# Performance work log

Hardware: AMD Instinct MI355X
Metric: run time of the kernel (lower is better)

Reference implementation:

```python
import jax, jax.numpy as jnp
import numpy as np

B, S, H = 2, 2048, 2048
NH, NKV, HD = 32, 8, 64
GROUPS = NH // NKV
SCALE = HD ** -0.5


def _rope_tables(key):
    # Real RoPE cos/sin tables (HF Llama style), shape [B, S, HD]
    inv_freq = 1.0 / (10000.0 ** (jnp.arange(0, HD, 2, dtype=jnp.float32) / HD))  # [HD/2]
    t = jnp.arange(S, dtype=jnp.float32)
    freqs = jnp.outer(t, inv_freq)                      # [S, HD/2]
    emb = jnp.concatenate([freqs, freqs], axis=-1)      # [S, HD]
    cos = jnp.broadcast_to(jnp.cos(emb)[None], (B, S, HD))
    sin = jnp.broadcast_to(jnp.sin(emb)[None], (B, S, HD))
    return cos, sin


def setup_inputs() -> dict:
    key = jax.random.key(0)
    ks = jax.random.split(key, 9)
    w = 0.02
    cos, sin = _rope_tables(key)
    return {
        "hidden_states": jax.random.normal(ks[0], (B, S, H), jnp.float32),
        "bounding_box_embeddings": jax.random.normal(ks[1], (B, S, H), jnp.float32),
        "cos": cos,
        "sin": sin,
        "Wq": jax.random.normal(ks[2], (H, NH * HD), jnp.float32) * w,
        "Wk": jax.random.normal(ks[3], (H, NKV * HD), jnp.float32) * w,
        "Wv": jax.random.normal(ks[4], (H, NKV * HD), jnp.float32) * w,
        "Wo": jax.random.normal(ks[5], (NH * HD, H), jnp.float32) * w,
        "Wsq": jax.random.normal(ks[6], (H, NH * HD), jnp.float32) * w,
        "Wsk": jax.random.normal(ks[7], (H, NKV * HD), jnp.float32) * w,
    }


def _rotate_half(x):
    x1, x2 = x[..., : HD // 2], x[..., HD // 2 :]
    return jnp.concatenate([-x2, x1], axis=-1)


def _apply_rope(q, k, cos, sin):
    # q: [B,NH,S,HD], k: [B,NKV,S,HD]; cos/sin [B,S,HD] -> broadcast over heads
    c = cos[:, None, :, :]
    s = sin[:, None, :, :]
    return q * c + _rotate_half(q) * s, k * c + _rotate_half(k) * s


def _proj_heads(x, W, n_heads):
    b, s, _ = x.shape
    return (x @ W).reshape(b, s, n_heads, HD).transpose(0, 2, 1, 3)  # [B,nh,S,HD]


def reference(hidden_states, bounding_box_embeddings, cos, sin, Wq, Wk, Wv, Wo, Wsq, Wsk):
    # Text Q/K/V with RoPE
    q = _proj_heads(hidden_states, Wq, NH)
    k = _proj_heads(hidden_states, Wk, NKV)
    v = _proj_heads(hidden_states, Wv, NKV)
    q, k = _apply_rope(q, k, cos, sin)
    # Spatial Q/K (no V) with RoPE
    sq = _proj_heads(bounding_box_embeddings, Wsq, NH)
    sk = _proj_heads(bounding_box_embeddings, Wsk, NKV)
    sq, sk = _apply_rope(sq, sk, cos, sin)
    # Fused text+spatial states, then GQA repeat_kv
    q = q + sq                                   # [B,NH,S,HD]
    k = jnp.repeat(k + sk, GROUPS, axis=1)       # [B,NH,S,HD]
    v = jnp.repeat(v, GROUPS, axis=1)            # [B,NH,S,HD]
    # Eager attention with causal mask
    scores = jnp.einsum("bhqd,bhkd->bhqk", q, k) * SCALE
    causal = jnp.tril(jnp.ones((S, S), dtype=bool))
    scores = jnp.where(causal[None, None], scores, jnp.finfo(jnp.float32).min)
    probs = jax.nn.softmax(scores.astype(jnp.float32), axis=-1).astype(q.dtype)
    attn = jnp.einsum("bhqk,bhkd->bhqd", probs, v)           # [B,NH,S,HD]
    attn = attn.transpose(0, 2, 1, 3).reshape(B, S, NH * HD)  # [B,S,NH*HD]
    return attn @ Wo
```

## Files before the change

### kernel.cpp

```cpp
#include <hip/hip_runtime.h>

#define B_ 2
#define S_ 2048
#define H_ 2048
#define NH_ 32
#define NKV_ 8
#define HD_ 64

typedef short short8 __attribute__((ext_vector_type(8)));
typedef float f32x4 __attribute__((ext_vector_type(4)));
typedef float f32x16 __attribute__((ext_vector_type(16)));
typedef unsigned int uint4v __attribute__((ext_vector_type(4)));

__device__ __forceinline__ float bf2f(unsigned short u) {
  union { unsigned int i; float f; } v; v.i = ((unsigned int)u) << 16; return v.f;
}
__device__ __forceinline__ unsigned short f2bf(float f) {
  union { float f; unsigned int i; } v; v.f = f;
  unsigned int u = v.i;
  u += 0x7fffu + ((u >> 16) & 1u);
  return (unsigned short)(u >> 16);
}
__device__ __forceinline__ unsigned int cvtpk(float lo, float hi) {
  unsigned int r;
  asm("v_cvt_pk_bf16_f32 %0, %1, %2" : "=v"(r) : "v"(lo), "v"(hi));
  return r;
}
__device__ __forceinline__ void pl32swap(unsigned int& a, unsigned int& b) {
  asm("v_permlane32_swap_b32 %0, %1" : "+v"(a), "+v"(b));
}
__device__ __forceinline__ short8 mkfrag(unsigned a, unsigned b, unsigned c, unsigned d) {
  union { uint4v u; short8 s; } x;
  x.u = (uint4v){a, b, c, d};
  return x.s;
}
__device__ __forceinline__ void gload_lds16(const unsigned short* g, unsigned short* l) {
  __builtin_amdgcn_global_load_lds((const __attribute__((address_space(1))) void*)g,
                                   (__attribute__((address_space(3))) void*)l,
                                   16, 0, 0);
}
#define MFMA32(A, B, C) __builtin_amdgcn_mfma_f32_32x32x16_bf16(A, B, C, 0, 0, 0)
#define BARF() asm volatile("s_barrier" ::: "memory")

__global__ __launch_bounds__(256) void castA_frag(const float* __restrict__ in,
                                                  unsigned short* __restrict__ out) {
  int c = blockIdx.x * 4 + (threadIdx.x >> 6);
  int l = threadIdx.x & 63;
  int D = c & 31, KT = (c >> 5) & 31, bm = c >> 10;
  int row = bm * 256 + ((D >> 4) & 1) * 128 + ((D >> 3) & 1) * 64 + ((D >> 1) & 3) * 16 + (l & 15);
  int k = KT * 64 + (D & 1) * 32 + (l >> 4) * 8;
  const float* src = in + (size_t)row * 2048 + k;
  float4 v0 = *(const float4*)src;
  float4 v1 = *(const float4*)(src + 4);
  ushort4 o0, o1;
  o0.x = f2bf(v0.x); o0.y = f2bf(v0.y); o0.z = f2bf(v0.z); o0.w = f2bf(v0.w);
  o1.x = f2bf(v1.x); o1.y = f2bf(v1.y); o1.z = f2bf(v1.z); o1.w = f2bf(v1.w);
  unsigned short* dst = out + (size_t)c * 512 + l * 8;
  *(ushort4*)dst = o0;
  *(ushort4*)(dst + 4) = o1;
}

__global__ __launch_bounds__(256) void castW_frag(const float* __restrict__ W0,
                                                  const float* __restrict__ W1,
                                                  const float* __restrict__ W2,
                                                  unsigned short* __restrict__ out) {
  __shared__ float tile[64][33];
  int c = blockIdx.x;
  int ngroup = c & 7, KT = (c >> 3) & 31, bn = c >> 8;
  int n0 = bn * 256 + ngroup * 32;
  const float* W; int Nw, nb;
  if (n0 < 2048)      { W = W0; Nw = 2048; nb = n0; }
  else if (n0 < 2560) { W = W1; Nw = 512;  nb = n0 - 2048; }
  else                { W = W2; Nw = 512;  nb = n0 - 2560; }
  int t = threadIdx.x;
  int col = t & 31, r8 = t >> 5;
#pragma unroll
  for (int p = 0; p < 8; ++p) {
    int kk = p * 8 + r8;
    tile[kk][col] = W[(size_t)(KT * 64 + kk) * Nw + nb + col];
  }
  __syncthreads();
  int e = t >> 6, l = t & 63;
  int nf = e >> 1, ks = e & 1;
  ushort4 o0, o1;
  unsigned short* op = (unsigned short*)&o0;
#pragma unroll
  for (int j = 0; j < 8; ++j) {
    unsigned short v = f2bf(tile[ks * 32 + (l >> 4) * 8 + j][nf * 16 + (l & 15)]);
    if (j < 4) op[j] = v; else ((unsigned short*)&o1)[j - 4] = v;
  }
  unsigned short* dst = out + (((size_t)(c >> 3) * 32 + ngroup * 4 + e) << 9) + l * 8;
  *(ushort4*)dst = o0;
  *(ushort4*)(dst + 4) = o1;
}

__global__ __launch_bounds__(256) void vtrans_kernel(const unsigned short* __restrict__ P1,
                                                     unsigned short* __restrict__ Vt) {
  __shared__ unsigned short tile[32][33];
  int s0 = blockIdx.x * 32, d0 = blockIdx.y * 32, bk = blockIdx.z;
  int b = bk >> 3, kv = bk & 7;
  int tx = threadIdx.x & 31, ty = threadIdx.x >> 5;
#pragma unroll
  for (int i = 0; i < 32; i += 8)
    tile[ty + i][tx] = P1[(size_t)(b * S_ + s0 + ty + i) * 3072 + 2560 + kv * 64 + d0 + tx];
  __syncthreads();
#pragma unroll
  for (int i = 0; i < 32; i += 8)
    Vt[(size_t)(bk * 64 + d0 + ty + i) * S_ + s0 + tx] = tile[tx][ty + i];
}

__global__ __launch_bounds__(256) void combine_rope(const unsigned short* __restrict__ P1,
                                                    const unsigned short* __restrict__ P2,
                                                    const float* __restrict__ cosT,
                                                    const float* __restrict__ sinT,
                                                    unsigned short* __restrict__ Qb,
                                                    unsigned short* __restrict__ Kb) {
  int id = blockIdx.x * 256 + threadIdx.x;
  int row = id / 640;
  int grp = id - row * 640;
  int b = row >> 11;
  int s = row & 2047;
  bool isQ = grp < 512;
  int n = isQ ? grp * 4 : (grp - 512) * 4;
  int h = n >> 6;
  int d = n & 63;
  int base = isQ ? 0 : 2048;
  const int ld1 = 3072, ld2 = 2560;
  int pd = (d < 32) ? d + 32 : d - 32;
  float sign = (d < 32) ? -1.f : 1.f;
  int pcol = base + h * 64 + pd;

  ushort4 a1 = *(const ushort4*)&P1[(size_t)row * ld1 + base + n];
  ushort4 a2 = *(const ushort4*)&P2[(size_t)row * ld2 + base + n];
  ushort4 b1 = *(const ushort4*)&P1[(size_t)row * ld1 + pcol];
  ushort4 b2 = *(const ushort4*)&P2[(size_t)row * ld2 + pcol];
  float4 cv = *(const float4*)&cosT[(size_t)row * 64 + d];
  float4 sv = *(const float4*)&sinT[(size_t)row * 64 + d];
  float scale = isQ ? 0.125f : 1.0f;

  float xs[4] = { bf2f(a1.x) + bf2f(a2.x), bf2f(a1.y) + bf2f(a2.y),
                  bf2f(a1.z) + bf2f(a2.z), bf2f(a1.w) + bf2f(a2.w) };
  float xp[4] = { bf2f(b1.x) + bf2f(b2.x), bf2f(b1.y) + bf2f(b2.y),
                  bf2f(b1.z) + bf2f(b2.z), bf2f(b1.w) + bf2f(b2.w) };
  float cc[4] = { cv.x, cv.y, cv.z, cv.w };
  float ss[4] = { sv.x, sv.y, sv.z, sv.w };
  ushort4 o;
  unsigned short* op = (unsigned short*)&o;
#pragma unroll
  for (int i = 0; i < 4; ++i)
    op[i] = f2bf((xs[i] * cc[i] + sign * xp[i] * ss[i]) * scale);

  if (isQ)
    *(ushort4*)&Qb[((size_t)(b * NH_ + h) * S_ + s) * HD_ + d] = o;
  else
    *(ushort4*)&Kb[((size_t)(b * NKV_ + h) * S_ + s) * HD_ + d] = o;
}

#define RD_A(BC, MH) do { \
  _Pragma("unroll") for (int mf = 0; mf < 4; ++mf) { \
    _Pragma("unroll") for (int ks = 0; ks < 2; ++ks) \
      a[mf][ks] = *(const short8*)&lds[BC][((wm * 2 + (MH)) * 8 + mf * 2 + ks) * 512 + l * 8]; \
  } \
} while (0)

#define RD_B(BC, NH, DST) do { \
  _Pragma("unroll") for (int nf = 0; nf < 2; ++nf) { \
    _Pragma("unroll") for (int ks = 0; ks < 2; ++ks) \
      DST[nf][ks] = *(const short8*)&lds[BC][16384 + (((wn * 2 + (NH)) * 2 + nf) * 2 + ks) * 512 + l * 8]; \
  } \
} while (0)

#define MM(MH, NH, BB) do { \
  _Pragma("unroll") for (int mf = 0; mf < 4; ++mf) { \
    _Pragma("unroll") for (int nf = 0; nf < 2; ++nf) { \
      _Pragma("unroll") for (int ks = 0; ks < 2; ++ks) \
        acc[(MH) * 4 + mf][(NH) * 2 + nf] = __builtin_amdgcn_mfma_f32_16x16x32_bf16( \
            a[mf][ks], BB[nf][ks], acc[(MH) * 4 + mf][(NH) * 2 + nf], 0, 0, 0); \
    } \
  } \
} while (0)

#define STAGE_A(H, KT) do { \
  int bq_ = (KT) & 1; \
  int d1_ = (H) * 8 + w; \
  gload_lds16(aF + (((size_t)((KT) * 32 + d1_)) << 9), &lds[bq_][d1_ * 512]); \
  gload_lds16(aF + (((size_t)((KT) * 32 + 16 + d1_)) << 9), &lds[bq_][(16 + d1_) * 512]); \
} while (0)

#define STAGE_B(H, KT) do { \
  int bq_ = (KT) & 1; \
  int e1_ = (w >> 2) * 8 + (H) * 4 + (w & 3); \
  gload_lds16(bF + (((size_t)((KT) * 32 + e1_)) << 9), &lds[bq_][16384 + e1_ * 512]); \
  gload_lds16(bF + (((size_t)((KT) * 32 + 16 + e1_)) << 9), &lds[bq_][16384 + (16 + e1_) * 512]); \
} while (0)

#define GROUP_P(BC, G) do { \
  int kt1 = (G) + 1; if (kt1 > 31) kt1 = 31; \
  int kt2 = (G) + 2; if (kt2 > 31) kt2 = 31; \
  int BN_ = kt1 & 1; \
  BARF(); \
  __builtin_amdgcn_s_setprio(1); MM(0, 0, b0); __builtin_amdgcn_s_setprio(0); \
  RD_B(BC, 1, b1); \
  STAGE_A(1, kt1); \
  BARF(); \
  __builtin_amdgcn_s_setprio(1); MM(0, 1, b1); __builtin_amdgcn_s_setprio(0); \
  STAGE_A(0, kt2); \
  BARF(); \
  RD_A(BC, 1); \
  __builtin_amdgcn_s_setprio(1); MM(1, 0, b0); __builtin_amdgcn_s_setprio(0); \
  STAGE_B(0, kt2); \
  asm volatile("s_waitcnt vmcnt(8)" ::: "memory"); \
  BARF(); \
  __builtin_amdgcn_s_setprio(1); MM(1, 1, b1); __builtin_amdgcn_s_setprio(0); \
  RD_A(BN_, 0); \
  RD_B(BN_, 0, b0); \
  STAGE_B(1, kt2); \
  asm volatile("s_waitcnt vmcnt(6)" ::: "memory"); \
} while (0)

__global__ __launch_bounds__(512, 2) void gemm256(const unsigned short* __restrict__ Afr,
                                                  const unsigned short* __restrict__ Wfr,
                                                  void* __restrict__ Cv,
                                                  int N, int nbx) {
  __shared__ unsigned short lds[2][32768];
  int nwg = gridDim.x;
  int orig = blockIdx.x;
  int wgid = (orig & 7) * (nwg >> 3) + (orig >> 3);
  int bn = wgid % nbx, bm = wgid / nbx;
  int t = threadIdx.x, w = t >> 6, l = t & 63;
  int wm = w >> 2, wn = w & 3;

  const unsigned short* aF = Afr + ((size_t)bm << 19) + l * 8;
  const unsigned short* bF = Wfr + ((size_t)bn << 19) + l * 8;

  short8 a[4][2], b0[2][2], b1[2][2];
  f32x4 acc[8][4];
#pragma unroll
  for (int mi = 0; mi < 8; ++mi)
#pragma unroll
    for (int ni = 0; ni < 4; ++ni) acc[mi][ni] = 0.f;

  STAGE_A(0, 0); STAGE_A(1, 0); STAGE_B(0, 0); STAGE_B(1, 0);
  STAGE_A(0, 1); STAGE_B(0, 1); STAGE_B(1, 1);
  asm volatile("s_waitcnt vmcnt(6)" ::: "memory");
  BARF();
  RD_A(0, 0);
  RD_B(0, 0, b0);

  for (int tg = 0; tg < 32; tg += 2) {
    GROUP_P(0, tg);
    GROUP_P(1, tg + 1);
  }
  asm volatile("s_waitcnt vmcnt(0)" ::: "memory");

#pragma unroll
  for (int mi = 0; mi < 8; ++mi) {
    int row = bm * 256 + wm * 128 + (mi >> 2) * 64 + (mi & 3) * 16 + (l >> 4) * 4;
#pragma unroll
    for (int ni = 0; ni < 4; ++ni) {
      int col = bn * 256 + wn * 64 + (ni >> 1) * 32 + (ni & 1) * 16 + (l & 15);
#pragma unroll
      for (int r = 0; r < 4; ++r)
        ((unsigned short*)Cv)[(size_t)(row + r) * N + col] = f2bf(acc[mi][ni][r]);
    }
  }
}

#define RD_AO(BC) do { \
  _Pragma("unroll") for (int mf = 0; mf < 4; ++mf) { \
    _Pragma("unroll") for (int ks = 0; ks < 2; ++ks) \
      a[mf][ks] = *(const short8*)&lds3[BC][(wm * 8 + mf * 2 + ks) * 512 + l * 8]; \
  } \
} while (0)

#define RD_BO(BC, NH, DST) do { \
  _Pragma("unroll") for (int nf = 0; nf < 2; ++nf) { \
    _Pragma("unroll") for (int ks = 0; ks < 2; ++ks) \
      DST[nf][ks] = *(const short8*)&lds3[BC][8192 + (((wn * 2 + (NH)) * 2 + nf) * 2 + ks) * 512 + l * 8]; \
  } \
} while (0)

#define MM_O(NH, BB) do { \
  _Pragma("unroll") for (int mf = 0; mf < 4; ++mf) { \
    _Pragma("unroll") for (int nf = 0; nf < 2; ++nf) { \
      _Pragma("unroll") for (int ks = 0; ks < 2; ++ks) \
        acc[mf][(NH) * 2 + nf] = __builtin_amdgcn_mfma_f32_16x16x32_bf16( \
            a[mf][ks], BB[nf][ks], acc[mf][(NH) * 2 + nf], 0, 0, 0); \
    } \
  } \
} while (0)

#define STAGE_AO(KT) do { \
  int bq_ = (KT) & 1; \
  gload_lds16(aRM + (size_t)(KT) * 64, &lds3[bq_][w * 512]); \
  gload_lds16(aRM + (size_t)64 * 2048 + (size_t)(KT) * 64, &lds3[bq_][(8 + w) * 512]); \
} while (0)

#define STAGE_BO(H, KT) do { \
  int bq_ = (KT) & 1; \
  int e1_ = (w >> 2) * 8 + (H) * 4 + (w & 3); \
  gload_lds16(bF + (((size_t)((KT) * 32 + e1_)) << 9), &lds3[bq_][8192 + e1_ * 512]); \
  gload_lds16(bF + (((size_t)((KT) * 32 + 16 + e1_)) << 9), &lds3[bq_][8192 + (16 + e1_) * 512]); \
} while (0)

#define GROUPO(BC, G) do { \
  int kt1 = (G) + 1; if (kt1 > 31) kt1 = 31; \
  int kt2 = (G) + 2; if (kt2 > 31) kt2 = 31; \
  RD_AO(BC); RD_BO(BC, 0, b0); \
  STAGE_BO(1, kt1); \
  BARF(); \
  __builtin_amdgcn_s_setprio(1); MM_O(0, b0); __builtin_amdgcn_s_setprio(0); \
  BARF(); \
  RD_BO(BC, 1, b1); \
  STAGE_AO(kt2); STAGE_BO(0, kt2); \
  BARF(); \
  __builtin_amdgcn_s_setprio(1); MM_O(1, b1); __builtin_amdgcn_s_setprio(0); \
  asm volatile("s_waitcnt vmcnt(4)" ::: "memory"); \
  BARF(); \
} while (0)

__global__ __launch_bounds__(512, 2) void gemm_op(const unsigned short* __restrict__ Arm,
                                                  const unsigned short* __restrict__ Wfr,
                                                  float* __restrict__ C,
                                                  int N, int nbx) {
  __shared__ unsigned short lds3[2][24576];
  int nwg = gridDim.x;
  int orig = blockIdx.x;
  int wgid = (orig & 7) * (nwg >> 3) + (orig >> 3);
  int bn = wgid % nbx, bm = wgid / nbx;
  int t = threadIdx.x, w = t >> 6, l = t & 63;
  int wm = w >> 2, wn = w & 3;

  const unsigned short* aRM = Arm +
      (size_t)(bm * 128 + ((w >> 1) & 3) * 16 + (l & 15)) * 2048 + (w & 1) * 32 + (l >> 4) * 8;
  const unsigned short* bF = Wfr + ((size_t)bn << 19) + l * 8;

  short8 a[4][2], b0[2][2], b1[2][2];
  f32x4 acc[4][4];
#pragma unroll
  for (int mi = 0; mi < 4; ++mi)
#pragma unroll
    for (int ni = 0; ni < 4; ++ni) acc[mi][ni] = 0.f;

  STAGE_AO(0); STAGE_BO(0, 0); STAGE_BO(1, 0);
  STAGE_AO(1); STAGE_BO(0, 1);
  asm volatile("s_waitcnt vmcnt(4)" ::: "memory");
  BARF();

  for (int tg = 0; tg < 32; tg += 2) {
    GROUPO(0, tg);
    GROUPO(1, tg + 1);
  }
  asm volatile("s_waitcnt vmcnt(0)" ::: "memory");

#pragma unroll
  for (int mf = 0; mf < 4; ++mf) {
    int row = bm * 128 + wm * 64 + mf * 16 + (l >> 4) * 4;
#pragma unroll
    for (int ni = 0; ni < 4; ++ni) {
      int col = bn * 256 + wn * 64 + (ni >> 1) * 32 + (ni & 1) * 16 + (l & 15);
#pragma unroll
      for (int r = 0; r < 4; ++r)
        C[(size_t)(row + r) * N + col] = acc[mf][ni][r];
    }
  }
}

__global__ __launch_bounds__(512) void attn_kernel(const unsigned short* __restrict__ Q,
                                                   const unsigned short* __restrict__ K,
                                                   const unsigned short* __restrict__ Vt,
                                                   unsigned short* __restrict__ attnOut) {
  __shared__ unsigned short lK[2][64 * 64];
  __shared__ unsigned short lV[2][64 * 64];

  int bx = blockIdx.x;
  int j = bx & 7;
  int bh = bx >> 3;
  int head = bh & 31;
  int b = bh >> 5;
  int kvh = head >> 2;
  const unsigned short* Kp = K + (size_t)(b * NKV_ + kvh) * S_ * HD_;
  const unsigned short* Vp = Vt + (size_t)(b * NKV_ + kvh) * HD_ * S_;

  int t = threadIdx.x;
  int w = t >> 6, l = t & 63;
  int q32 = l & 31, hf = l >> 5;
  int qb_eff = (w < 4) ? j : (15 - j);
  int qbase_w = qb_eff * 128 + (w & 3) * 32;
  const unsigned short* Qp = Q + ((size_t)(b * NH_ + head) * S_ + qbase_w) * HD_;

  short8 qf[4];
  {
    const unsigned short* qrow = Qp + (size_t)q32 * HD_ + hf * 8;
#pragma unroll
    for (int kc = 0; kc < 4; ++kc)
      qf[kc] = *(const short8*)(qrow + kc * 16);
  }

  int srow = t >> 3;
  int sslot = t & 7;
  unsigned lOff = srow * 128 + ((sslot ^ (srow & 7)) << 4);
  const char* gK0 = (const char*)(Kp + (size_t)srow * 64 + sslot * 8);
  const char* gV0 = (const char*)(Vp + (size_t)srow * 2048 + sslot * 8);

  {
    int4 rk = *(const int4*)(gK0);
    int4 rv = *(const int4*)(gV0);
    *(int4*)((char*)lK[0] + lOff) = rk;
    *(int4*)((char*)lV[0] + lOff) = rv;
  }
  __syncthreads();

  f32x16 oA = 0.f, oB = 0.f;
  float mrun = -1e30f, lrun = 0.f;

  int nt = 32 - 2 * j;
  int cur = 0;
  for (int tI = 0; tI < nt; ++tI) {
    int kv0 = tI * 64;
    bool pf = (tI + 1 < nt);
    int4 nk, nv;
    if (pf) {
      nk = *(const int4*)(gK0 + (size_t)(kv0 + 64) * 128);
      nv = *(const int4*)(gV0 + (size_t)(kv0 + 64) * 2);
    }

    if (kv0 <= qbase_w + 31) {
      const char* lKc = (const char*)lK[cur];
      const char* lVc = (const char*)lV[cur];
      int swz = q32 & 7;

      f32x16 sA = 0.f, sB = 0.f;
      __builtin_amdgcn_s_setprio(1);
#pragma unroll
      for (int kc = 0; kc < 4; ++kc) {
        int cs = (kc << 1) | hf;
        short8 ak0 = *(const short8*)(lKc + q32 * 128 + ((cs ^ swz) << 4));
        short8 ak1 = *(const short8*)(lKc + (32 + q32) * 128 + ((cs ^ swz) << 4));
        sA = MFMA32(ak0, qf[kc], sA);
        sB = MFMA32(ak1, qf[kc], sB);
      }
      __builtin_amdgcn_s_setprio(0);

      if (kv0 + 63 > qbase_w) {
        int qg = qbase_w + q32;
#pragma unroll
        for (int r = 0; r < 16; ++r) {
          int kvr = kv0 + (r & 3) + ((r >> 2) << 3) + (hf << 2);
          if (kvr > qg) sA[r] = -1e30f;
          if (kvr + 32 > qg) sB[r] = -1e30f;
        }
      }

      float pmax = sA[0];
#pragma unroll
      for (int r = 1; r < 16; ++r) pmax = fmaxf(pmax, sA[r]);
#pragma unroll
      for (int r = 0; r < 16; ++r) pmax = fmaxf(pmax, sB[r]);
      pmax = fmaxf(pmax, __shfl_xor(pmax, 32, 64));

      if (!__all(pmax <= mrun + 8.f)) {
        float mnew = fmaxf(mrun, pmax);
        float sf = __expf(mrun - mnew);
        lrun *= sf;
        mrun = mnew;
#pragma unroll
        for (int r = 0; r < 16; ++r) {
          int src = (r & 3) + ((r >> 2) << 3) + (hf << 2);
          float sfr = __shfl(sf, src, 64);
          oA[r] *= sfr;
          oB[r] *= sfr;
        }
      }

      float rs = 0.f;
#pragma unroll
      for (int r = 0; r < 16; ++r) { sA[r] = __expf(sA[r] - mrun); rs += sA[r]; }
#pragma unroll
      for (int r = 0; r < 16; ++r) { sB[r] = __expf(sB[r] - mrun); rs += sB[r]; }
      rs += __shfl_xor(rs, 32, 64);
      lrun += rs;

      short8 paf[4];
      {
        unsigned c0 = cvtpk(sA[0], sA[1]), c1 = cvtpk(sA[2], sA[3]);
        unsigned c2 = cvtpk(sA[4], sA[5]), c3 = cvtpk(sA[6], sA[7]);
        pl32swap(c0, c2); pl32swap(c1, c3);
        paf[0] = mkfrag(c0, c1, c2, c3);
      }
      {
        unsigned c0 = cvtpk(sA[8], sA[9]),  c1 = cvtpk(sA[10], sA[11]);
        unsigned c2 = cvtpk(sA[12], sA[13]), c3 = cvtpk(sA[14], sA[15]);
        pl32swap(c0, c2); pl32swap(c1, c3);
        paf[1] = mkfrag(c0, c1, c2, c3);
      }
      {
        unsigned c0 = cvtpk(sB[0], sB[1]), c1 = cvtpk(sB[2], sB[3]);
        unsigned c2 = cvtpk(sB[4], sB[5]), c3 = cvtpk(sB[6], sB[7]);
        pl32swap(c0, c2); pl32swap(c1, c3);
        paf[2] = mkfrag(c0, c1, c2, c3);
      }
      {
        unsigned c0 = cvtpk(sB[8], sB[9]),  c1 = cvtpk(sB[10], sB[11]);
        unsigned c2 = cvtpk(sB[12], sB[13]), c3 = cvtpk(sB[14], sB[15]);
        pl32swap(c0, c2); pl32swap(c1, c3);
        paf[3] = mkfrag(c0, c1, c2, c3);
      }

      __builtin_amdgcn_s_setprio(1);
#pragma unroll
      for (int ks = 0; ks < 4; ++ks) {
        int cs = (ks << 1) | hf;
        short8 v0 = *(const short8*)(lVc + q32 * 128 + ((cs ^ swz) << 4));
        short8 v1 = *(const short8*)(lVc + (32 + q32) * 128 + ((cs ^ swz) << 4));
        oA = MFMA32(paf[ks], v0, oA);
        oB = MFMA32(paf[ks], v1, oB);
      }
      __builtin_amdgcn_s_setprio(0);
    }

    if (pf) {
      *(int4*)((char*)lK[cur ^ 1] + lOff) = nk;
      *(int4*)((char*)lV[cur ^ 1] + lOff) = nv;
    }
    __syncthreads();
    cur ^= 1;
  }

  float linv = 1.f / lrun;
#pragma unroll
  for (int r = 0; r < 16; ++r) {
    int src = (r & 3) + ((r >> 2) << 3) + (hf << 2);
    float li = __shfl(linv, src, 64);
    unsigned short* op = attnOut + ((size_t)(b * S_ + qbase_w + src)) * (NH_ * HD_) + head * 64;
    op[q32] = f2bf(oA[r] * li);
    op[32 + q32] = f2bf(oB[r] * li);
  }
}

extern "C" void kernel_launch(void* const* d_in, const int* in_sizes, int n_in,
                              void* d_out, int out_size, void* d_ws, size_t ws_size,
                              hipStream_t stream) {
  const float* hidden = (const float*)d_in[0];
  const float* bbox   = (const float*)d_in[1];
  const float* cosT   = (const float*)d_in[2];
  const float* sinT   = (const float*)d_in[3];
  const float* Wq  = (const float*)d_in[4];
  const float* Wk  = (const float*)d_in[5];
  const float* Wv  = (const float*)d_in[6];
  const float* Wo  = (const float*)d_in[7];
  const float* Wsq = (const float*)d_in[8];
  const float* Wsk = (const float*)d_in[9];

  char* ws = (char*)d_ws;
  size_t off = 0;
  auto alloc = [&](size_t bytes) {
    void* p = ws + off;
    off += (bytes + 255) & ~(size_t)255;
    return p;
  };
  unsigned short* AfrH = (unsigned short*)alloc((size_t)4096 * 2048 * 2);
  unsigned short* AfrB = (unsigned short*)alloc((size_t)4096 * 2048 * 2);
  unsigned short* WhF  = (unsigned short*)alloc((size_t)3072 * 2048 * 2);
  unsigned short* WbF  = (unsigned short*)alloc((size_t)2560 * 2048 * 2);
  unsigned short* WoF  = (unsigned short*)alloc((size_t)2048 * 2048 * 2);
  unsigned short* P1   = (unsigned short*)alloc((size_t)4096 * 3072 * 2);
  unsigned short* P2   = (unsigned short*)alloc((size_t)4096 * 2560 * 2);
  unsigned short* Qb     = AfrB;
  unsigned short* Kb     = AfrH;
  unsigned short* Vt     = AfrH + (size_t)B_ * NKV_ * S_ * HD_;
  unsigned short* attnRM = WhF;

  dim3 blk(256);
  castA_frag<<<dim3(4096), blk, 0, stream>>>(hidden, AfrH);
  castA_frag<<<dim3(4096), blk, 0, stream>>>(bbox,   AfrB);
  castW_frag<<<dim3(3072), blk, 0, stream>>>(Wq,  Wk,  Wv,      WhF);
  castW_frag<<<dim3(2560), blk, 0, stream>>>(Wsq, Wsk, nullptr, WbF);
  castW_frag<<<dim3(2048), blk, 0, stream>>>(Wo,  Wo,  Wo,      WoF);

  gemm256<<<dim3(192), dim3(512), 0, stream>>>(AfrH, WhF, P1, 3072, 12);
  gemm256<<<dim3(160), dim3(512), 0, stream>>>(AfrB, WbF, P2, 2560, 10);

  combine_rope<<<dim3((B_ * S_ * 640) / 256), blk, 0, stream>>>(P1, P2, cosT, sinT, Qb, Kb);
  vtrans_kernel<<<dim3(64, 2, 16), blk, 0, stream>>>(P1, Vt);

  attn_kernel<<<dim3(512), dim3(512), 0, stream>>>(Qb, Kb, Vt, attnRM);

  gemm_op<<<dim3(256), dim3(512), 0, stream>>>(attnRM, WoF, (float*)d_out, 2048, 8);
}
```

Before: 250.2 us.

## Split attention blocks into single query tiles scheduled longest-first

The attention kernel previously paired a short and a long causal query block in one 512-thread workgroup so every workgroup had equal work. It now launches 1024 workgroups of 256 threads, each handling one 128-row query block, ordered from the longest KV range to the shortest so the hardware scheduler can balance load dynamically. Each thread now stages two 16-byte chunks per K/V tile instead of one. The aim is smaller workgroups and higher occupancy with no warps idling on masked tiles, at the cost of more K/V tile loads per query row and more barriers.

```diff
diff --git a/kernel.cpp b/kernel.cpp
--- a/kernel.cpp
+++ b/kernel.cpp
@@ -366,7 +366,7 @@
   }
 }
 
-__global__ __launch_bounds__(512) void attn_kernel(const unsigned short* __restrict__ Q,
+__global__ __launch_bounds__(256) void attn_kernel(const unsigned short* __restrict__ Q,
                                                    const unsigned short* __restrict__ K,
                                                    const unsigned short* __restrict__ Vt,
                                                    unsigned short* __restrict__ attnOut) {
@@ -374,10 +374,10 @@
   __shared__ unsigned short lV[2][64 * 64];
 
   int bx = blockIdx.x;
-  int j = bx & 7;
-  int bh = bx >> 3;
-  int head = bh & 31;
-  int b = bh >> 5;
+  int qb = 15 - (bx >> 6);
+  int hh = bx & 63;
+  int head = hh & 31;
+  int b = hh >> 5;
   int kvh = head >> 2;
   const unsigned short* Kp = K + (size_t)(b * NKV_ + kvh) * S_ * HD_;
   const unsigned short* Vp = Vt + (size_t)(b * NKV_ + kvh) * HD_ * S_;
@@ -385,8 +385,7 @@
   int t = threadIdx.x;
   int w = t >> 6, l = t & 63;
   int q32 = l & 31, hf = l >> 5;
-  int qb_eff = (w < 4) ? j : (15 - j);
-  int qbase_w = qb_eff * 128 + (w & 3) * 32;
+  int qbase_w = qb * 128 + w * 32;
   const unsigned short* Qp = Q + ((size_t)(b * NH_ + head) * S_ + qbase_w) * HD_;
 
   short8 qf[4];
@@ -397,32 +396,39 @@
       qf[kc] = *(const short8*)(qrow + kc * 16);
   }
 
-  int srow = t >> 3;
-  int sslot = t & 7;
-  unsigned lOff = srow * 128 + ((sslot ^ (srow & 7)) << 4);
-  const char* gK0 = (const char*)(Kp + (size_t)srow * 64 + sslot * 8);
-  const char* gV0 = (const char*)(Vp + (size_t)srow * 2048 + sslot * 8);
+  int srow = t >> 2;
+  int ss0 = t & 3;
+  unsigned lOff0 = srow * 128 + ((ss0 ^ (srow & 7)) << 4);
+  unsigned lOff1 = srow * 128 + (((ss0 + 4) ^ (srow & 7)) << 4);
+  const char* gK0 = (const char*)(Kp + (size_t)srow * 64 + ss0 * 8);
+  const char* gV0 = (const char*)(Vp + (size_t)srow * 2048 + ss0 * 8);
 
   {
-    int4 rk = *(const int4*)(gK0);
-    int4 rv = *(const int4*)(gV0);
-    *(int4*)((char*)lK[0] + lOff) = rk;
-    *(int4*)((char*)lV[0] + lOff) = rv;
+    int4 rk0 = *(const int4*)(gK0);
+    int4 rk1 = *(const int4*)(gK0 + 64);
+    int4 rv0 = *(const int4*)(gV0);
+    int4 rv1 = *(const int4*)(gV0 + 64);
+    *(int4*)((char*)lK[0] + lOff0) = rk0;
+    *(int4*)((char*)lK[0] + lOff1) = rk1;
+    *(int4*)((char*)lV[0] + lOff0) = rv0;
+    *(int4*)((char*)lV[0] + lOff1) = rv1;
   }
   __syncthreads();
 
   f32x16 oA = 0.f, oB = 0.f;
   float mrun = -1e30f, lrun = 0.f;
 
-  int nt = 32 - 2 * j;
+  int nt = 2 * qb + 2;
   int cur = 0;
   for (int tI = 0; tI < nt; ++tI) {
     int kv0 = tI * 64;
     bool pf = (tI + 1 < nt);
-    int4 nk, nv;
+    int4 nk0, nk1, nv0, nv1;
     if (pf) {
-      nk = *(const int4*)(gK0 + (size_t)(kv0 + 64) * 128);
-      nv = *(const int4*)(gV0 + (size_t)(kv0 + 64) * 2);
+      nk0 = *(const int4*)(gK0 + (size_t)(kv0 + 64) * 128);
+      nk1 = *(const int4*)(gK0 + (size_t)(kv0 + 64) * 128 + 64);
+      nv0 = *(const int4*)(gV0 + (size_t)(kv0 + 64) * 2);
+      nv1 = *(const int4*)(gV0 + (size_t)(kv0 + 64) * 2 + 64);
     }
 
     if (kv0 <= qbase_w + 31) {
@@ -520,8 +526,10 @@
     }
 
     if (pf) {
-      *(int4*)((char*)lK[cur ^ 1] + lOff) = nk;
-      *(int4*)((char*)lV[cur ^ 1] + lOff) = nv;
+      *(int4*)((char*)lK[cur ^ 1] + lOff0) = nk0;
+      *(int4*)((char*)lK[cur ^ 1] + lOff1) = nk1;
+      *(int4*)((char*)lV[cur ^ 1] + lOff0) = nv0;
+      *(int4*)((char*)lV[cur ^ 1] + lOff1) = nv1;
     }
     __syncthreads();
     cur ^= 1;
@@ -584,7 +592,7 @@
   combine_rope<<<dim3((B_ * S_ * 640) / 256), blk, 0, stream>>>(P1, P2, cosT, sinT, Qb, Kb);
   vtrans_kernel<<<dim3(64, 2, 16), blk, 0, stream>>>(P1, Vt);
 
-  attn_kernel<<<dim3(512), dim3(512), 0, stream>>>(Qb, Kb, Vt, attnRM);
+  attn_kernel<<<dim3(1024), dim3(256), 0, stream>>>(Qb, Kb, Vt, attnRM);
 
   gemm_op<<<dim3(256), dim3(512), 0, stream>>>(attnRM, WoF, (float*)d_out, 2048, 8);
 }
```

Result: slower. 261.9 us (+4.7%).
